# Optimization experiments

Hardware: AMD Instinct MI355X
Metric: run time of the kernel (lower is better)

The kernel has to match this reference:

```python
import jax, jax.numpy as jnp
import numpy as np

B, S, F_IN = 8, 4096, 256      # batch, frames, mel bins
C = 256                        # model_complexity (out_features of attention)
G = 8                          # n_heads (groups)
K = 31                         # w_size (local window, odd)
F_OUT = 88                     # output_features (piano keys)
PAD = (K - 1) // 2


def setup_inputs() -> dict:
    key = jax.random.key(0)
    ks = jax.random.split(key, 7)
    s = 0.05
    return {
        "spec": jax.random.normal(ks[0], (B, S, F_IN), jnp.float32),
        "W_q": jax.random.normal(ks[1], (F_IN, C), jnp.float32) * s,
        "W_k": jax.random.normal(ks[2], (F_IN, C), jnp.float32) * s,
        "W_v": jax.random.normal(ks[3], (F_IN, C), jnp.float32) * s,
        "rel": jax.random.normal(ks[4], (C, K), jnp.float32),
        "W_lin": jax.random.normal(ks[5], (C, F_OUT), jnp.float32) * s,
        "b_lin": jax.random.normal(ks[6], (F_OUT,), jnp.float32) * s,
    }


def reference(spec, W_q, W_k, W_v, rel, W_lin, b_lin):
    b, s, _ = spec.shape
    d = C // G  # per-head dim
    # QKV projections (no bias, as in the module)
    q = spec @ W_q                                             # [B,S,C]
    padded = jnp.pad(spec, ((0, 0), (PAD, PAD), (0, 0)))       # [B,S+2p,F]
    k = padded @ W_k                                           # [B,S+2p,C]
    v = padded @ W_v
    # unfold: window index [S,K]
    idx = jnp.arange(s)[:, None] + jnp.arange(K)[None, :]      # [S,K]
    kw = jnp.transpose(k[:, idx, :], (0, 1, 3, 2))             # [B,S,C,K]
    vw = jnp.transpose(v[:, idx, :], (0, 1, 3, 2))             # [B,S,C,K]
    kw = kw + rel                                              # positional bias [C,K]
    kw = kw.reshape(b, s, G, d, K)
    vw = vw.reshape(b, s, G, d, K)
    qh = q.reshape(b, s, G, d)
    energy = jnp.einsum('bsgd,bsgdk->bsgk', qh, kw)            # [B,S,G,K]
    attn = jax.nn.softmax(energy, axis=-1)                     # [B,S,G,K]
    out = jnp.einsum('bsgk,bsgdk->bsgd', attn, vw).reshape(b, s, C)
    frame_pred = jax.nn.sigmoid(out @ W_lin + b_lin)           # [B,S,F_OUT]
    return frame_pred, attn
```

## Files before the change

### kernel.cpp

```cpp
#include <hip/hip_runtime.h>
#include <hip/hip_bf16.h>
#include <math.h>

#define B_   8
#define S_   4096
#define FIN  256
#define C_   256
#define G_   8
#define D_   32
#define K_   31
#define PAD_ 15
#define FOUT 88

typedef __bf16 bf16;
typedef __attribute__((ext_vector_type(8))) __bf16 bf16x8;
typedef __attribute__((ext_vector_type(4))) __bf16 bf16x4;
typedef __attribute__((ext_vector_type(4))) float f32x4;

#define MFMA16(A, B, C) __builtin_amdgcn_mfma_f32_16x16x32_bf16(A, B, C, 0, 0, 0)

__global__ __launch_bounds__(256) void prep_all(
    const float* __restrict__ Wq, const float* __restrict__ Wk,
    const float* __restrict__ Wv, const float* __restrict__ Wl,
    const float* __restrict__ rel,
    bf16* __restrict__ bth, bf16* __restrict__ btl,
    bf16* __restrict__ wlh, bf16* __restrict__ wll,
    bf16* __restrict__ Vt,
    bf16* __restrict__ relH, bf16* __restrict__ relL)
{
    const int bid = blockIdx.x;
    const int t   = threadIdx.x;

    if (bid < 768) {
        const int w = bid >> 8;
        const int k = bid & 255;
        const float* W = (w == 0) ? Wq : (w == 1) ? Wk : Wv;
        const float x = W[(size_t)k * 256 + t];
        const bf16 h = (bf16)x;
        const size_t o = (size_t)w * 65536 + (size_t)t * 256 + k;
        bth[o] = h;
        btl[o] = (bf16)(x - (float)h);
    } else if (bid < 896) {
        const int k = (bid - 768) * 2 + (t >> 7);
        const int n = t & 127;
        const float x = (n < FOUT) ? Wl[(size_t)k * FOUT + n] : 0.f;
        const bf16 h = (bf16)x;
        wlh[(size_t)n * 256 + k] = h;
        wll[(size_t)n * 256 + k] = (bf16)(x - (float)h);
    } else if (bid < 1024) {
        const int idx = (bid - 896) * 256 + t;
        const int bd  = idx >> 4;
        const int pos = (idx & 15) * 4;
        const int off = (pos < 16) ? pos : 4096 + pos;
        bf16x4 z = {};
        *(bf16x4*)&Vt[(size_t)bd * 4160 + off] = z;
    } else {
        const int idx = (bid - 1024) * 256 + t;
        const int g = idx >> 10, k = (idx >> 5) & 31, d = idx & 31;
        const float v = (k < 31) ? rel[(size_t)(g * 32 + d) * 31 + k] : 0.f;
        const bf16 h = (bf16)v;
        relH[idx] = h;
        relL[idx] = (bf16)(v - (float)h);
    }
}

__device__ __forceinline__ void gload16(const bf16* g, bf16* l) {
    __builtin_amdgcn_global_load_lds(
        (const __attribute__((address_space(1))) void*)g,
        (__attribute__((address_space(3))) void*)l, 16, 0, 0);
}

__device__ __forceinline__ void stage_tile(const bf16* g, bf16* l, int t) {
    const int lg = ((t & 3) ^ ((t >> 3) & 3)) * 8;
    const int r0 = t >> 2;
    const int r1 = 64 + (t >> 2);
    const int u0 = (t & ~63) * 8;
    gload16(g + (size_t)r0 * 256 + lg, l + u0);
    gload16(g + (size_t)r1 * 256 + lg, l + u0 + 2048);
}

__device__ __forceinline__ bf16x8 frag_ld(const bf16* l, int r, int cl) {
    return *(const bf16x8*)&l[r * 32 + ((cl ^ ((r >> 1) & 3)) << 3)];
}

__global__ __launch_bounds__(256) void qkv_mfma(
    const float* __restrict__ spec,
    const bf16* __restrict__ bth, const bf16* __restrict__ btl,
    bf16* __restrict__ Qh, bf16* __restrict__ Ql,
    bf16* __restrict__ Kh, bf16* __restrict__ Kl,
    bf16* __restrict__ Vt)
{
    __shared__ bf16 lds[6 * 4096];

    const int t   = threadIdx.x;
    const int swz = ((blockIdx.x & 7) * 192) + (blockIdx.x >> 3);
    const int mt  = swz / 6, nt = swz % 6;
    const int wt  = nt >> 1;
    const int m0  = mt * 128, n0 = (nt & 1) * 128;
    const bool three = (wt < 2);

    const float* a_g = spec + (size_t)m0 * 256;
    const bf16* bh_g = bth + (size_t)wt * 65536 + (size_t)n0 * 256;
    const bf16* bl_g = btl + (size_t)wt * 65536 + (size_t)n0 * 256;

    const int ar  = t >> 1;
    const int ak  = (t & 1) * 16;
    const int as_ = (ar >> 1) & 3;
    const int cc0 = ak >> 3;
    bf16* AhW0 = lds +        ar * 32 + (( cc0      ^ as_) << 3);
    bf16* AhW1 = lds +        ar * 32 + (((cc0 + 1) ^ as_) << 3);
    bf16* AlW0 = lds + 4096 + ar * 32 + (( cc0      ^ as_) << 3);
    bf16* AlW1 = lds + 4096 + ar * 32 + (((cc0 + 1) ^ as_) << 3);
    const float* aRow = a_g + (size_t)ar * 256 + ak;

    const int lane = t & 63, wid = t >> 6;
    const int wr = (wid >> 1) * 64, wc = (wid & 1) * 64;
    const int fr = lane & 15, cl = lane >> 4;

    f32x4 acc[4][4];
#pragma unroll
    for (int m = 0; m < 4; ++m)
#pragma unroll
        for (int n = 0; n < 4; ++n)
            acc[m][n] = (f32x4){0.f, 0.f, 0.f, 0.f};

    stage_tile(bh_g, lds + 8192, t);
    stage_tile(bl_g, lds + 12288, t);
    f32x4 a0 = *(const f32x4*)(aRow);
    f32x4 a1 = *(const f32x4*)(aRow + 4);
    f32x4 a2 = *(const f32x4*)(aRow + 8);
    f32x4 a3 = *(const f32x4*)(aRow + 12);

    for (int ks = 0; ks < 8; ++ks) {
        const int cur = ks & 1;
        bf16* Bcur = lds + 8192 + cur * 8192;

        f32x4 n0_, n1_, n2_, n3_;
        if (ks < 7) {
            bf16* Bnxt = lds + 8192 + (cur ^ 1) * 8192;
            const int ko2 = (ks + 1) * 32;
            stage_tile(bh_g + ko2, Bnxt, t);
            stage_tile(bl_g + ko2, Bnxt + 4096, t);
            n0_ = *(const f32x4*)(aRow + ko2);
            n1_ = *(const f32x4*)(aRow + ko2 + 4);
            n2_ = *(const f32x4*)(aRow + ko2 + 8);
            n3_ = *(const f32x4*)(aRow + ko2 + 12);
        }

        bf16x8 h0, h1, l0, l1;
#pragma unroll
        for (int j = 0; j < 4; ++j) {
            const bf16 x0 = (bf16)a0[j], x1 = (bf16)a1[j];
            const bf16 x2 = (bf16)a2[j], x3 = (bf16)a3[j];
            h0[j] = x0; h0[4 + j] = x1;
            h1[j] = x2; h1[4 + j] = x3;
            l0[j]     = (bf16)(a0[j] - (float)x0);
            l0[4 + j] = (bf16)(a1[j] - (float)x1);
            l1[j]     = (bf16)(a2[j] - (float)x2);
            l1[4 + j] = (bf16)(a3[j] - (float)x3);
        }
        *(bf16x8*)AhW0 = h0;
        *(bf16x8*)AhW1 = h1;
        if (three) {
            *(bf16x8*)AlW0 = l0;
            *(bf16x8*)AlW1 = l1;
        }

        asm volatile("s_waitcnt vmcnt(8) lgkmcnt(0)" ::: "memory");
        __builtin_amdgcn_s_barrier();

        bf16x8 ah[4], bh8[4], bl8[4];
#pragma unroll
        for (int m = 0; m < 4; ++m) ah[m] = frag_ld(lds, wr + m * 16 + fr, cl);
#pragma unroll
        for (int n = 0; n < 4; ++n) {
            bh8[n] = frag_ld(Bcur,        wc + n * 16 + fr, cl);
            bl8[n] = frag_ld(Bcur + 4096, wc + n * 16 + fr, cl);
        }
#pragma unroll
        for (int m = 0; m < 4; ++m)
#pragma unroll
            for (int n = 0; n < 4; ++n) {
                acc[m][n] = MFMA16(ah[m], bh8[n], acc[m][n]);
                acc[m][n] = MFMA16(ah[m], bl8[n], acc[m][n]);
            }
        if (three) {
            bf16x8 al[4];
#pragma unroll
            for (int m = 0; m < 4; ++m) al[m] = frag_ld(lds + 4096, wr + m * 16 + fr, cl);
#pragma unroll
            for (int m = 0; m < 4; ++m)
#pragma unroll
                for (int n = 0; n < 4; ++n)
                    acc[m][n] = MFMA16(al[m], bh8[n], acc[m][n]);
        }

        if (ks < 7) {
            __builtin_amdgcn_s_barrier();
            a0 = n0_; a1 = n1_; a2 = n2_; a3 = n3_;
        }
    }

    if (wt < 2) {
        bf16* Oh = (wt == 0) ? Qh : Kh;
        bf16* Ol = (wt == 0) ? Ql : Kl;
#pragma unroll
        for (int m = 0; m < 4; ++m) {
            const int gr = m0 + wr + m * 16 + cl * 4;
#pragma unroll
            for (int n = 0; n < 4; ++n) {
                const int gc = n0 + wc + n * 16 + fr;
#pragma unroll
                for (int i = 0; i < 4; ++i) {
                    const float v = acc[m][n][i];
                    const bf16 hh = (bf16)v;
                    const size_t off = (size_t)(gr + i) * 256 + gc;
                    Oh[off] = hh;
                    Ol[off] = (bf16)(v - (float)hh);
                }
            }
        }
    } else {
#pragma unroll
        for (int m = 0; m < 4; ++m) {
            const int gr = m0 + wr + m * 16 + cl * 4;
            const int bb = gr >> 12, sr = gr & 4095;
#pragma unroll
            for (int n = 0; n < 4; ++n) {
                const int gc = n0 + wc + n * 16 + fr;
                bf16x4 pk;
#pragma unroll
                for (int i = 0; i < 4; ++i) pk[i] = (bf16)acc[m][n][i];
                *(bf16x4*)&Vt[(size_t)(bb * 256 + gc) * 4160 + 16 + sr] = pk;
            }
        }
    }
}

__global__ __launch_bounds__(256) void attn_mfma(
    const bf16* __restrict__ Qh, const bf16* __restrict__ Ql,
    const bf16* __restrict__ Kh, const bf16* __restrict__ Kl,
    const bf16* __restrict__ Vt,
    const bf16* __restrict__ relH, const bf16* __restrict__ relL,
    float* __restrict__ attn, bf16* __restrict__ Obf)
{
    __shared__ char ldsb[18432];

    const int t    = threadIdx.x;
    const int wid  = t >> 6;
    const int lane = t & 63;
    const int fr   = lane & 15;
    const int q    = lane >> 4;
    const int f7   = fr & 7;
    const int sl   = lane >> 2;
    const int jj   = lane & 3;

    const int bid2 = ((blockIdx.x & 7) << 8) | (blockIdx.x >> 3);
    const int sg0  = bid2 << 4;
    const int b    = sg0 >> 12;
    const int s0   = sg0 & 4095;

    float* Rbuf = (float*)(ldsb + wid * 4608);
    float* Pf32 = Rbuf;
    bf16*  Pbuf = (bf16*) (ldsb + wid * 4608 + 2304);

    {
        uint* p32 = (uint*)Pbuf;
#pragma unroll
        for (int j = 0; j < 9; ++j) p32[lane + 64 * j] = 0u;
    }

    const size_t rowQ = (size_t)(sg0 + fr) * 256;

#pragma unroll
    for (int h = 0; h < 2; ++h) {
        asm volatile("" ::: "memory");
        const int g   = wid * 2 + h;
        const int dof = g * 32 + q * 8;

        const bf16x8 qh8 = *(const bf16x8*)&Qh[rowQ + dof];
        const bf16x8 ql8 = *(const bf16x8*)&Ql[rowQ + dof];

        f32x4 e0, e1, e2;
#pragma unroll
        for (int tau = 0; tau < 3; ++tau) {
            const int trel = s0 - 16 + tau * 16 + fr;
            bf16x8 kh8 = {}, kl8 = {};
            if ((unsigned)trel < 4096u) {
                const size_t rk = ((size_t)(b << 12) + trel) * 256 + dof;
                kh8 = *(const bf16x8*)&Kh[rk];
                kl8 = *(const bf16x8*)&Kl[rk];
            }
            f32x4 a = (f32x4){0.f, 0.f, 0.f, 0.f};
            a = MFMA16(kh8, qh8, a);
            a = MFMA16(kh8, ql8, a);
            a = MFMA16(kl8, qh8, a);
            if (tau == 0) e0 = a; else if (tau == 1) e1 = a; else e2 = a;
        }

#pragma unroll
        for (int kap = 0; kap < 2; ++kap) {
            const size_t ro = (size_t)(g * 32 + kap * 16 + fr) * 32 + q * 8;
            const bf16x8 rh8 = *(const bf16x8*)&relH[ro];
            const bf16x8 rl8 = *(const bf16x8*)&relL[ro];
            f32x4 rc = (f32x4){0.f, 0.f, 0.f, 0.f};
            rc = MFMA16(rh8, qh8, rc);
            rc = MFMA16(rh8, ql8, rc);
            rc = MFMA16(rl8, qh8, rc);
#pragma unroll
            for (int r = 0; r < 4; ++r)
                Rbuf[(kap * 16 + q * 4 + r) * 18 + fr] = rc[r];
        }

        float ev[3][4];
        float mx = -3.0e38f;
#pragma unroll
        for (int tau = 0; tau < 3; ++tau) {
#pragma unroll
            for (int r = 0; r < 4; ++r) {
                const int rp = q * 4 + r;
                const int kk = tau * 16 + rp - fr - 1;
                const float eb = (tau == 0) ? e0[r] : (tau == 1) ? e1[r] : e2[r];
                float v = eb + Rbuf[(kk & 31) * 18 + fr];
                const bool valid = (tau == 1) || ((tau == 0) ? (rp > fr) : (rp < fr));
                v = valid ? v : -3.0e38f;
                ev[tau][r] = v;
                mx = fmaxf(mx, v);
            }
        }
        mx = fmaxf(mx, __shfl_xor(mx, 16));
        mx = fmaxf(mx, __shfl_xor(mx, 32));
        float sum = 0.f;
#pragma unroll
        for (int tau = 0; tau < 3; ++tau)
#pragma unroll
            for (int r = 0; r < 4; ++r) {
                const float p = __expf(ev[tau][r] - mx);
                ev[tau][r] = p;
                sum += p;
            }
        sum += __shfl_xor(sum, 16);
        sum += __shfl_xor(sum, 32);
        const float inv = 1.f / sum;

#pragma unroll
        for (int tau = 0; tau < 3; ++tau)
#pragma unroll
            for (int r = 0; r < 4; ++r) {
                const int rp = q * 4 + r;
                const int kk = tau * 16 + rp - fr - 1;
                const bool valid = (tau == 1) || ((tau == 0) ? (rp > fr) : (rp < fr));
                if (valid) {
                    const float p = ev[tau][r] * inv;
                    Pf32[fr * 36 + kk] = p;
                    const int tl = tau * 16 + rp;
                    Pbuf[fr * 72 + (((tl >> 3) ^ f7) << 3) + (tl & 7)] = (bf16)p;
                }
            }

        asm volatile("" ::: "memory");
        {
            float* arow = &attn[((size_t)(sg0 + sl) * 8 + g) * 31];
#pragma unroll
            for (int i = 0; i < 8; ++i) {
                const int k = jj + 4 * i;
                if (k < 31) arow[k] = Pf32[sl * 36 + k];
            }
        }

        asm volatile("" ::: "memory");
        const bf16x8 pa0 = *(const bf16x8*)&Pbuf[fr * 72 + ((q ^ f7) << 3)];
        const bf16x8 pa1 = *(const bf16x8*)&Pbuf[fr * 72 + (((4 + q) ^ f7) << 3)];
#pragma unroll
        for (int dl = 0; dl < 2; ++dl) {
            const size_t vrow = (size_t)(b * 256 + g * 32 + dl * 16 + fr) * 4160
                              + s0 + q * 8;
            const bf16x8 v0 = *(const bf16x8*)&Vt[vrow];
            const bf16x8 v1 = *(const bf16x8*)&Vt[vrow + 32];
            f32x4 o = (f32x4){0.f, 0.f, 0.f, 0.f};
            o = MFMA16(v0, pa0, o);
            o = MFMA16(v1, pa1, o);
            bf16x4 pk;
#pragma unroll
            for (int r = 0; r < 4; ++r) pk[r] = (bf16)o[r];
            *(bf16x4*)&Obf[(size_t)(sg0 + fr) * 256 + g * 32 + dl * 16 + (q << 2)] = pk;
        }
    }
}

__global__ __launch_bounds__(256) void frame_mfma(
    const bf16* __restrict__ O,
    const bf16* __restrict__ wlh, const bf16* __restrict__ wll,
    const float* __restrict__ bl, float* __restrict__ frame)
{
    __shared__ bf16 lds[3 * 4096];

    const int t  = threadIdx.x;
    const int m0 = blockIdx.x * 128;

    const bf16* a_g = O + (size_t)m0 * 256;

    const int lane = t & 63, wid = t >> 6;
    const int wr = (wid >> 1) * 64, wc = (wid & 1) * 64;
    const int fr = lane & 15, cl = lane >> 4;

    f32x4 acc[4][4];
#pragma unroll
    for (int m = 0; m < 4; ++m)
#pragma unroll
        for (int n = 0; n < 4; ++n)
            acc[m][n] = (f32x4){0.f, 0.f, 0.f, 0.f};

    for (int ks = 0; ks < 8; ++ks) {
        const int ko = ks * 32;
        stage_tile(a_g + ko, lds, t);
        stage_tile(wlh + ko, lds + 4096, t);
        stage_tile(wll + ko, lds + 8192, t);
        __syncthreads();

        bf16x8 ah[4], bh8[4], bl4[4];
#pragma unroll
        for (int m = 0; m < 4; ++m) ah[m] = frag_ld(lds, wr + m * 16 + fr, cl);
#pragma unroll
        for (int n = 0; n < 4; ++n) {
            bh8[n] = frag_ld(lds + 4096, wc + n * 16 + fr, cl);
            bl4[n] = frag_ld(lds + 8192, wc + n * 16 + fr, cl);
        }
#pragma unroll
        for (int m = 0; m < 4; ++m)
#pragma unroll
            for (int n = 0; n < 4; ++n) {
                acc[m][n] = MFMA16(ah[m], bh8[n], acc[m][n]);
                acc[m][n] = MFMA16(ah[m], bl4[n], acc[m][n]);
            }
        __syncthreads();
    }

#pragma unroll
    for (int m = 0; m < 4; ++m) {
        const int gr = m0 + wr + m * 16 + cl * 4;
#pragma unroll
        for (int n = 0; n < 4; ++n) {
            const int gc = wc + n * 16 + fr;
            if (gc < FOUT) {
                const float bb = bl[gc];
#pragma unroll
                for (int i = 0; i < 4; ++i) {
                    const float x = acc[m][n][i] + bb;
                    frame[(size_t)(gr + i) * FOUT + gc] = 1.f / (1.f + __expf(-x));
                }
            }
        }
    }
}

extern "C" void kernel_launch(void* const* d_in, const int* in_sizes, int n_in,
                              void* d_out, int out_size, void* d_ws, size_t ws_size,
                              hipStream_t stream) {
    (void)in_sizes; (void)n_in; (void)out_size; (void)ws_size;
    const float* spec = (const float*)d_in[0];
    const float* Wq   = (const float*)d_in[1];
    const float* Wk   = (const float*)d_in[2];
    const float* Wv   = (const float*)d_in[3];
    const float* rel  = (const float*)d_in[4];
    const float* Wl   = (const float*)d_in[5];
    const float* bl   = (const float*)d_in[6];

    float* frame = (float*)d_out;
    float* attn  = frame + (size_t)B_ * S_ * FOUT;

    bf16* bth  = (bf16*)((char*)d_out + 33554432);
    bf16* btl  = bth + 3 * 65536;

    bf16* Qh   = (bf16*)d_ws;
    bf16* Ql   = Qh + (size_t)8388608;
    bf16* Kh   = Ql + (size_t)8388608;
    bf16* Kl   = Kh + (size_t)8388608;
    bf16* Vt   = Kl + (size_t)8388608;
    bf16* wlh  = Vt + (size_t)8 * 256 * 4160;
    bf16* wll  = wlh + 128 * 256;
    bf16* relH = wll + 128 * 256;
    bf16* relL = relH + 8192;

    prep_all  <<<dim3(1056), 256, 0, stream>>>(Wq, Wk, Wv, Wl, rel,
                                               bth, btl, wlh, wll, Vt, relH, relL);
    qkv_mfma  <<<dim3(1536), 256, 0, stream>>>(spec, bth, btl, Qh, Ql, Kh, Kl, Vt);
    attn_mfma <<<dim3(2048), 256, 0, stream>>>(Qh, Ql, Kh, Kl, Vt, relH, relL, attn, Qh);
    frame_mfma<<<dim3(256),  256, 0, stream>>>(Qh, wlh, wll, bl, frame);
}
```

Before: 110.6 us.

## Store K as fp32 and split in attention; stage Q epilogue through LDS

The QKV kernel now writes K as a single fp32 tensor instead of separate bf16 hi/lo tensors, and the attention kernel does the hi/lo bf16 split on the fly after loading. The Q hi/lo epilogue is staged through LDS so each wave writes coalesced 16-byte rows instead of scattered 2-byte stores. Bytes written for K stay the same, but it becomes one stream of 4-byte stores instead of two of 2-byte stores. Attention gains extra conversion ALU work per K load and extra LDS round trips in the epilogue.

```diff
diff --git a/kernel.cpp b/kernel.cpp
--- a/kernel.cpp
+++ b/kernel.cpp
@@ -87,7 +87,7 @@
     const float* __restrict__ spec,
     const bf16* __restrict__ bth, const bf16* __restrict__ btl,
     bf16* __restrict__ Qh, bf16* __restrict__ Ql,
-    bf16* __restrict__ Kh, bf16* __restrict__ Kl,
+    float* __restrict__ Kf,
     bf16* __restrict__ Vt)
 {
     __shared__ bf16 lds[6 * 4096];
@@ -201,9 +201,36 @@
         }
     }
 
-    if (wt < 2) {
-        bf16* Oh = (wt == 0) ? Qh : Kh;
-        bf16* Ol = (wt == 0) ? Ql : Kl;
+    __syncthreads();
+
+    if (wt == 0) {
+        bf16* tb = lds + wid * 4224;
+#pragma unroll
+        for (int p = 0; p < 2; ++p) {
+            bf16* Out = (p == 0) ? Qh : Ql;
+#pragma unroll
+            for (int m = 0; m < 4; ++m)
+#pragma unroll
+                for (int n = 0; n < 4; ++n)
+#pragma unroll
+                    for (int i = 0; i < 4; ++i) {
+                        const float v = acc[m][n][i];
+                        const bf16 hh = (bf16)v;
+                        tb[(m * 16 + cl * 4 + i) * 66 + n * 16 + fr] =
+                            (p == 0) ? hh : (bf16)(v - (float)hh);
+                    }
+            asm volatile("s_waitcnt lgkmcnt(0)" ::: "memory");
+#pragma unroll
+            for (int j = 0; j < 8; ++j) {
+                const int rr = j * 8 + (lane >> 3);
+                const int cc = (lane & 7) * 8;
+                const bf16x8 vv = *(const bf16x8*)&tb[rr * 66 + cc];
+                *(bf16x8*)&Out[(size_t)(m0 + wr + rr) * 256 + n0 + wc + cc] = vv;
+            }
+            if (p == 0)
+                asm volatile("s_waitcnt lgkmcnt(0)" ::: "memory");
+        }
+    } else if (wt == 1) {
 #pragma unroll
         for (int m = 0; m < 4; ++m) {
             const int gr = m0 + wr + m * 16 + cl * 4;
@@ -211,13 +238,8 @@
             for (int n = 0; n < 4; ++n) {
                 const int gc = n0 + wc + n * 16 + fr;
 #pragma unroll
-                for (int i = 0; i < 4; ++i) {
-                    const float v = acc[m][n][i];
-                    const bf16 hh = (bf16)v;
-                    const size_t off = (size_t)(gr + i) * 256 + gc;
-                    Oh[off] = hh;
-                    Ol[off] = (bf16)(v - (float)hh);
-                }
+                for (int i = 0; i < 4; ++i)
+                    Kf[(size_t)(gr + i) * 256 + gc] = acc[m][n][i];
             }
         }
     } else {
@@ -239,7 +261,7 @@
 
 __global__ __launch_bounds__(256) void attn_mfma(
     const bf16* __restrict__ Qh, const bf16* __restrict__ Ql,
-    const bf16* __restrict__ Kh, const bf16* __restrict__ Kl,
+    const float* __restrict__ Kf,
     const bf16* __restrict__ Vt,
     const bf16* __restrict__ relH, const bf16* __restrict__ relL,
     float* __restrict__ attn, bf16* __restrict__ Obf)
@@ -288,8 +310,16 @@
             bf16x8 kh8 = {}, kl8 = {};
             if ((unsigned)trel < 4096u) {
                 const size_t rk = ((size_t)(b << 12) + trel) * 256 + dof;
-                kh8 = *(const bf16x8*)&Kh[rk];
-                kl8 = *(const bf16x8*)&Kl[rk];
+                const f32x4 kA = *(const f32x4*)&Kf[rk];
+                const f32x4 kB = *(const f32x4*)&Kf[rk + 4];
+#pragma unroll
+                for (int j = 0; j < 4; ++j) {
+                    const bf16 hA = (bf16)kA[j];
+                    const bf16 hB = (bf16)kB[j];
+                    kh8[j] = hA; kh8[4 + j] = hB;
+                    kl8[j]     = (bf16)(kA[j] - (float)hA);
+                    kl8[4 + j] = (bf16)(kB[j] - (float)hB);
+                }
             }
             f32x4 a = (f32x4){0.f, 0.f, 0.f, 0.f};
             a = MFMA16(kh8, qh8, a);
@@ -472,19 +502,18 @@
     bf16* bth  = (bf16*)((char*)d_out + 33554432);
     bf16* btl  = bth + 3 * 65536;
 
-    bf16* Qh   = (bf16*)d_ws;
-    bf16* Ql   = Qh + (size_t)8388608;
-    bf16* Kh   = Ql + (size_t)8388608;
-    bf16* Kl   = Kh + (size_t)8388608;
-    bf16* Vt   = Kl + (size_t)8388608;
-    bf16* wlh  = Vt + (size_t)8 * 256 * 4160;
-    bf16* wll  = wlh + 128 * 256;
-    bf16* relH = wll + 128 * 256;
-    bf16* relL = relH + 8192;
+    bf16*  Qh   = (bf16*)d_ws;
+    bf16*  Ql   = Qh + (size_t)8388608;
+    float* Kf   = (float*)((char*)d_ws + 33554432);
+    bf16*  Vt   = (bf16*)((char*)d_ws + 67108864);
+    bf16*  wlh  = Vt + (size_t)8 * 256 * 4160;
+    bf16*  wll  = wlh + 128 * 256;
+    bf16*  relH = wll + 128 * 256;
+    bf16*  relL = relH + 8192;
 
     prep_all  <<<dim3(1056), 256, 0, stream>>>(Wq, Wk, Wv, Wl, rel,
                                                bth, btl, wlh, wll, Vt, relH, relL);
-    qkv_mfma  <<<dim3(1536), 256, 0, stream>>>(spec, bth, btl, Qh, Ql, Kh, Kl, Vt);
-    attn_mfma <<<dim3(2048), 256, 0, stream>>>(Qh, Ql, Kh, Kl, Vt, relH, relL, attn, Qh);
+    qkv_mfma  <<<dim3(1536), 256, 0, stream>>>(spec, bth, btl, Qh, Ql, Kf, Vt);
+    attn_mfma <<<dim3(2048), 256, 0, stream>>>(Qh, Ql, Kf, Vt, relH, relL, attn, Qh);
     frame_mfma<<<dim3(256),  256, 0, stream>>>(Qh, wlh, wll, bl, frame);
 }
```

New measurement: 115.6 us. +4.5%, slower.

## Double-buffer the A tile in LDS and cut to one barrier per k-step

Applied to the files above, without the earlier changes.

Adds a second LDS buffer for the bf16 hi/lo split A tile so the next step's A conversion and store happen after the MFMAs of the current step. This removes the second barrier per iteration, and the prefetched A and B loads overlap with compute. In exchange, LDS use grows from 48KB to 64KB per block, which may lower occupancy. The wait now drains all vmcnt before the barrier, which may expose global-load latency at the end of each step.

```diff
diff --git a/kernel.cpp b/kernel.cpp
--- a/kernel.cpp
+++ b/kernel.cpp
@@ -90,7 +90,7 @@
     bf16* __restrict__ Kh, bf16* __restrict__ Kl,
     bf16* __restrict__ Vt)
 {
-    __shared__ bf16 lds[6 * 4096];
+    __shared__ bf16 lds[8 * 4096];
 
     const int t   = threadIdx.x;
     const int swz = ((blockIdx.x & 7) * 192) + (blockIdx.x >> 3);
@@ -103,14 +103,12 @@
     const bf16* bh_g = bth + (size_t)wt * 65536 + (size_t)n0 * 256;
     const bf16* bl_g = btl + (size_t)wt * 65536 + (size_t)n0 * 256;
 
-    const int ar  = t >> 1;
-    const int ak  = (t & 1) * 16;
-    const int as_ = (ar >> 1) & 3;
-    const int cc0 = ak >> 3;
-    bf16* AhW0 = lds +        ar * 32 + (( cc0      ^ as_) << 3);
-    bf16* AhW1 = lds +        ar * 32 + (((cc0 + 1) ^ as_) << 3);
-    bf16* AlW0 = lds + 4096 + ar * 32 + (( cc0      ^ as_) << 3);
-    bf16* AlW1 = lds + 4096 + ar * 32 + (((cc0 + 1) ^ as_) << 3);
+    const int ar   = t >> 1;
+    const int ak   = (t & 1) * 16;
+    const int as_  = (ar >> 1) & 3;
+    const int cc0  = ak >> 3;
+    const int awo0 = ar * 32 + (( cc0      ^ as_) << 3);
+    const int awo1 = ar * 32 + (((cc0 + 1) ^ as_) << 3);
     const float* aRow = a_g + (size_t)ar * 256 + ak;
 
     const int lane = t & 63, wid = t >> 6;
@@ -124,29 +122,13 @@
         for (int n = 0; n < 4; ++n)
             acc[m][n] = (f32x4){0.f, 0.f, 0.f, 0.f};
 
-    stage_tile(bh_g, lds + 8192, t);
-    stage_tile(bl_g, lds + 12288, t);
-    f32x4 a0 = *(const f32x4*)(aRow);
-    f32x4 a1 = *(const f32x4*)(aRow + 4);
-    f32x4 a2 = *(const f32x4*)(aRow + 8);
-    f32x4 a3 = *(const f32x4*)(aRow + 12);
-
-    for (int ks = 0; ks < 8; ++ks) {
-        const int cur = ks & 1;
-        bf16* Bcur = lds + 8192 + cur * 8192;
-
-        f32x4 n0_, n1_, n2_, n3_;
-        if (ks < 7) {
-            bf16* Bnxt = lds + 8192 + (cur ^ 1) * 8192;
-            const int ko2 = (ks + 1) * 32;
-            stage_tile(bh_g + ko2, Bnxt, t);
-            stage_tile(bl_g + ko2, Bnxt + 4096, t);
-            n0_ = *(const f32x4*)(aRow + ko2);
-            n1_ = *(const f32x4*)(aRow + ko2 + 4);
-            n2_ = *(const f32x4*)(aRow + ko2 + 8);
-            n3_ = *(const f32x4*)(aRow + ko2 + 12);
-        }
-
+    {
+        f32x4 a0 = *(const f32x4*)(aRow);
+        f32x4 a1 = *(const f32x4*)(aRow + 4);
+        f32x4 a2 = *(const f32x4*)(aRow + 8);
+        f32x4 a3 = *(const f32x4*)(aRow + 12);
+        stage_tile(bh_g, lds + 16384, t);
+        stage_tile(bl_g, lds + 20480, t);
         bf16x8 h0, h1, l0, l1;
 #pragma unroll
         for (int j = 0; j < 4; ++j) {
@@ -159,19 +141,36 @@
             l1[j]     = (bf16)(a2[j] - (float)x2);
             l1[4 + j] = (bf16)(a3[j] - (float)x3);
         }
-        *(bf16x8*)AhW0 = h0;
-        *(bf16x8*)AhW1 = h1;
+        *(bf16x8*)&lds[awo0] = h0;
+        *(bf16x8*)&lds[awo1] = h1;
         if (three) {
-            *(bf16x8*)AlW0 = l0;
-            *(bf16x8*)AlW1 = l1;
-        }
-
-        asm volatile("s_waitcnt vmcnt(8) lgkmcnt(0)" ::: "memory");
+            *(bf16x8*)&lds[4096 + awo0] = l0;
+            *(bf16x8*)&lds[4096 + awo1] = l1;
+        }
+        asm volatile("s_waitcnt vmcnt(0) lgkmcnt(0)" ::: "memory");
         __builtin_amdgcn_s_barrier();
+    }
+
+    for (int ks = 0; ks < 8; ++ks) {
+        const int cur = ks & 1;
+        const int nxt = cur ^ 1;
+        bf16* Acur = lds + cur * 8192;
+        bf16* Bcur = lds + 16384 + cur * 8192;
+
+        f32x4 n0_, n1_, n2_, n3_;
+        if (ks < 7) {
+            const int ko2 = (ks + 1) * 32;
+            n0_ = *(const f32x4*)(aRow + ko2);
+            n1_ = *(const f32x4*)(aRow + ko2 + 4);
+            n2_ = *(const f32x4*)(aRow + ko2 + 8);
+            n3_ = *(const f32x4*)(aRow + ko2 + 12);
+            stage_tile(bh_g + ko2, lds + 16384 + nxt * 8192, t);
+            stage_tile(bl_g + ko2, lds + 20480 + nxt * 8192, t);
+        }
 
         bf16x8 ah[4], bh8[4], bl8[4];
 #pragma unroll
-        for (int m = 0; m < 4; ++m) ah[m] = frag_ld(lds, wr + m * 16 + fr, cl);
+        for (int m = 0; m < 4; ++m) ah[m] = frag_ld(Acur, wr + m * 16 + fr, cl);
 #pragma unroll
         for (int n = 0; n < 4; ++n) {
             bh8[n] = frag_ld(Bcur,        wc + n * 16 + fr, cl);
@@ -187,7 +186,7 @@
         if (three) {
             bf16x8 al[4];
 #pragma unroll
-            for (int m = 0; m < 4; ++m) al[m] = frag_ld(lds + 4096, wr + m * 16 + fr, cl);
+            for (int m = 0; m < 4; ++m) al[m] = frag_ld(Acur + 4096, wr + m * 16 + fr, cl);
 #pragma unroll
             for (int m = 0; m < 4; ++m)
 #pragma unroll
@@ -196,8 +195,27 @@
         }
 
         if (ks < 7) {
+            bf16* Anx = lds + nxt * 8192;
+            bf16x8 h0, h1, l0, l1;
+#pragma unroll
+            for (int j = 0; j < 4; ++j) {
+                const bf16 x0 = (bf16)n0_[j], x1 = (bf16)n1_[j];
+                const bf16 x2 = (bf16)n2_[j], x3 = (bf16)n3_[j];
+                h0[j] = x0; h0[4 + j] = x1;
+                h1[j] = x2; h1[4 + j] = x3;
+                l0[j]     = (bf16)(n0_[j] - (float)x0);
+                l0[4 + j] = (bf16)(n1_[j] - (float)x1);
+                l1[j]     = (bf16)(n2_[j] - (float)x2);
+                l1[4 + j] = (bf16)(n3_[j] - (float)x3);
+            }
+            *(bf16x8*)&Anx[awo0] = h0;
+            *(bf16x8*)&Anx[awo1] = h1;
+            if (three) {
+                *(bf16x8*)&Anx[4096 + awo0] = l0;
+                *(bf16x8*)&Anx[4096 + awo1] = l1;
+            }
+            asm volatile("s_waitcnt vmcnt(0) lgkmcnt(0)" ::: "memory");
             __builtin_amdgcn_s_barrier();
-            a0 = n0_; a1 = n1_; a2 = n2_; a3 = n3_;
         }
     }
 
```

Result: slower. 113.1 us (+2.2%).
